# Kernel optimization log

Hardware: AMD Instinct MI355X
Metric: run time of the kernel (lower is better)

The kernel has to match this reference:

```python
import jax, jax.numpy as jnp
from jax import lax
import numpy as np
import math

B = 8
DIFF_LEN, HORIZON, NUM_NODES = 336, 96, 1024
SEG_LEN, D_CONV, D_MODEL = 8, 64, 128
NUM_KERNELS, DEPTH, ALPHA = 6, 2, 0.05
FREQ = math.ceil(DIFF_LEN / SEG_LEN)      # 42
STEP = math.ceil(HORIZON / SEG_LEN)       # 12
PAD = SEG_LEN * FREQ - DIFF_LEN           # 0 here, code stays general
MAXK = 2 * NUM_KERNELS - 1                # 11


def setup_inputs() -> dict:
    key = jax.random.key(0)
    ks = iter(jax.random.split(key, 64))
    p = lambda *s: 0.02 * jax.random.normal(next(ks), s, jnp.float32)
    inp = dict(
        x_diff=jax.random.normal(next(ks), (B, DIFF_LEN, NUM_NODES), jnp.float32),
        adj=jax.random.uniform(next(ks), (NUM_NODES, NUM_NODES), jnp.float32),
        enc_w1=p(SEG_LEN, D_MODEL), enc_b1=p(D_MODEL),
        enc_w2=p(D_MODEL, D_CONV), enc_b2=p(D_CONV),
        dec_w1=p(D_CONV, D_MODEL), dec_b1=p(D_MODEL),
        dec_w2=p(D_MODEL, SEG_LEN), dec_b2=p(SEG_LEN),
        g1_w=p((DEPTH + 1) * D_CONV, D_CONV), g1_b=p(D_CONV),
        g2_w=p((DEPTH + 1) * D_CONV, D_CONV), g2_b=p(D_CONV),
    )
    for i in range(NUM_KERNELS):
        inp[f'conv_w{i}'] = p(D_CONV, D_CONV, 1, 2 * i + 1)
        inp[f'conv_b{i}'] = p(D_CONV)
    return inp


def _mlp(x, w1, b1, w2, b2):
    # 2-hidden-layer MLP with ReLU (dropout = identity at eval)
    return jnp.maximum(x @ w1 + b1, 0.0) @ w2 + b2


def _t_inception(x, conv_ws, conv_bs):
    # x: (B, D, N, T); inception = mean of 'same'-padded (1, 2i+1) convs
    out = jnp.zeros_like(x)
    for i, (w, b) in enumerate(zip(conv_ws, conv_bs)):
        out = out + lax.conv_general_dilated(
            x, w, (1, 1), ((0, 0), (i, i)),
            dimension_numbers=('NCHW', 'OIHW', 'NCHW')) + b[None, :, None, None]
    return out / len(conv_ws)


def _norm_adj(adj):
    a = adj + jnp.eye(adj.shape[0], dtype=adj.dtype)
    return a / a.sum(1, keepdims=True)


def _mixprop(x, a, w, b):
    # x: (B, T, N, D), a: row-normalized (N, N)
    h = x
    outs = [h]
    for _ in range(DEPTH):
        h = ALPHA * x + (1.0 - ALPHA) * jnp.einsum('vn,btnd->btvd', a, h)
        outs.append(h)
    return jnp.concatenate(outs, -1) @ w + b


def _stconv(x, a1, a2, conv_ws, conv_bs, g1_w, g1_b, g2_w, g2_b):
    res = jnp.transpose(x, (0, 3, 2, 1))            # b d n t
    res = _t_inception(res, conv_ws, conv_bs)
    res = jnp.transpose(res, (0, 3, 2, 1))          # b t n d
    res = _mixprop(res, a1, g1_w, g1_b) + _mixprop(res, a2, g2_w, g2_b)
    return res + x                                   # dropout = identity at eval


def reference(x_diff, adj,
              enc_w1, enc_b1, enc_w2, enc_b2,
              dec_w1, dec_b1, dec_w2, dec_b2,
              g1_w, g1_b, g2_w, g2_b,
              conv_w0, conv_b0, conv_w1, conv_b1, conv_w2, conv_b2,
              conv_w3, conv_b3, conv_w4, conv_b4, conv_w5, conv_b5):
    conv_ws = [conv_w0, conv_w1, conv_w2, conv_w3, conv_w4, conv_w5]
    conv_bs = [conv_b0, conv_b1, conv_b2, conv_b3, conv_b4, conv_b5]
    Bb, L, N = x_diff.shape
    a1 = _norm_adj(adj)
    a2 = _norm_adj(adj.T)

    # segment + left-pad with tail so length = FREQ * SEG_LEN
    res = jnp.concatenate((x_diff[:, L - PAD:, :], x_diff), axis=1)
    res = res.reshape(Bb, FREQ, SEG_LEN, N)
    res = jnp.transpose(res, (0, 1, 3, 2))          # (B, F, N, P)
    res = _mlp(res, enc_w1, enc_b1, enc_w2, enc_b2)  # (B, F, N, D)

    # reconstruction branch (teacher-forced one-step shift)
    rec = jnp.concatenate(
        (res[:, :1],
         _stconv(res[:, :-1], a1, a2, conv_ws, conv_bs, g1_w, g1_b, g2_w, g2_b)),
        axis=1)
    rec = _mlp(rec, dec_w1, dec_b1, dec_w2, dec_b2)  # (B, F, N, P)
    rec = jnp.transpose(rec, (0, 1, 3, 2)).reshape(Bb, FREQ * SEG_LEN, N)
    rec = rec[:, -DIFF_LEN:, :]

    cur = res[:, -MAXK:]                             # (B, MAXK, N, D)
    preds = []
    for _ in range(STEP):
        p = _stconv(cur, a1, a2, conv_ws, conv_bs, g1_w, g1_b, g2_w, g2_b)[:, -1:]
        preds.append(p)
        cur = jnp.concatenate((cur[:, 1:], p), axis=1)
    pred = jnp.concatenate(preds, axis=1)            # (B, STEP, N, D)
    pred = _mlp(pred, dec_w1, dec_b1, dec_w2, dec_b2)  # (B, STEP, N, SEG)
    # NOTE: original torch code does a raw .reshape (not transpose); replicate it
    pred = pred.reshape(Bb, STEP * SEG_LEN, N)[:, :HORIZON, :]
    return (rec, pred)
```

## Files before the change

### kernel.cpp

```cpp
#include <hip/hip_runtime.h>

typedef __bf16 bf16;
typedef __bf16 bf16x8 __attribute__((ext_vector_type(8)));
typedef float f32x4 __attribute__((ext_vector_type(4)));

#define N_NODES 1024
#define DC 64
#define FREQ 42
#define TREC 41
#define NB 8
#define MAXK 11
#define NSTEP 12
#define SLICE 65536

__global__ void transpose_k(const float* __restrict__ in, float* __restrict__ out) {
  __shared__ float tile[32][33];
  int bx = blockIdx.x * 32, by = blockIdx.y * 32;
  int x = threadIdx.x, y = threadIdx.y;
#pragma unroll
  for (int j = 0; j < 32; j += 8) tile[y + j][x] = in[(size_t)(by + y + j) * N_NODES + bx + x];
  __syncthreads();
#pragma unroll
  for (int j = 0; j < 32; j += 8) out[(size_t)(bx + y + j) * N_NODES + by + x] = tile[x][y + j];
}

__global__ void rowsum_k(const float* __restrict__ m, float* __restrict__ sums) {
  int v = blockIdx.x;
  float s = 0.f;
  for (int n = threadIdx.x; n < N_NODES; n += 256) s += m[(size_t)v * N_NODES + n];
  __shared__ float red[256];
  red[threadIdx.x] = s;
  __syncthreads();
  for (int w = 128; w > 0; w >>= 1) {
    if (threadIdx.x < w) red[threadIdx.x] += red[threadIdx.x + w];
    __syncthreads();
  }
  if (threadIdx.x == 0) sums[v] = red[0] + 1.0f;
}

__global__ void norm_k(const float* __restrict__ adj, const float* __restrict__ adjT,
                       const float* __restrict__ rs, const float* __restrict__ cs,
                       bf16* __restrict__ a1, bf16* __restrict__ a2) {
  int v = blockIdx.x & (N_NODES - 1);
  bool second = blockIdx.x >= N_NODES;
  const float* src = second ? adjT : adj;
  float inv = 1.0f / (second ? cs[v] : rs[v]);
  bf16* dst = second ? a2 : a1;
  for (int n = threadIdx.x; n < N_NODES; n += 256) {
    float val = src[(size_t)v * N_NODES + n] + (n == v ? 1.0f : 0.0f);
    dst[(size_t)v * N_NODES + n] = (bf16)(val * inv);
  }
}

__global__ __launch_bounds__(256) void btrans_k(const bf16* __restrict__ src,
                                                bf16* __restrict__ dst) {
  __shared__ __align__(16) bf16 t[64][72];
  int bx = blockIdx.x * 64, by = blockIdx.y * 64;
  int tid = threadIdx.x;
#pragma unroll
  for (int i = 0; i < 2; ++i) {
    int q = tid + i * 256;
    int r = q >> 3, c = (q & 7) * 8;
    *(uint4*)&t[r][c] = *(const uint4*)&src[(size_t)(by + r) * N_NODES + bx + c];
  }
  __syncthreads();
#pragma unroll
  for (int i = 0; i < 2; ++i) {
    int q = tid + i * 256;
    int rr = q >> 3, cc = (q & 7) * 8;
    bf16 tmp[8];
#pragma unroll
    for (int e = 0; e < 8; ++e) tmp[e] = t[cc + e][rr];
    *(uint4*)&dst[(size_t)(bx + rr) * N_NODES + by + cc] = *(uint4*)tmp;
  }
}

__global__ void combine_w_k(const float* w0, const float* w1, const float* w2, const float* w3,
                            const float* w4, const float* w5, const float* b0, const float* b1,
                            const float* b2, const float* b3, const float* b4, const float* b5,
                            bf16* __restrict__ Wc, float* __restrict__ bsum) {
  int idx = blockIdx.x * 256 + threadIdx.x;
  if (idx < MAXK * 4096) {
    int dtI = idx >> 12;
    int dout = (idx >> 6) & 63;
    int di = idx & 63;
    int d = dtI - 5;
    int ad = d < 0 ? -d : d;
    const float* ws[6] = {w0, w1, w2, w3, w4, w5};
    float s = 0.f;
    for (int i = 0; i < 6; ++i)
      if (i >= ad) {
        int K = 2 * i + 1;
        s += ws[i][((size_t)dout * 64 + di) * K + (d + i)];
      }
    Wc[idx] = (bf16)s;
  }
  if (idx < 64) bsum[idx] = b0[idx] + b1[idx] + b2[idx] + b3[idx] + b4[idx] + b5[idx];
}

__global__ void vt_k(const float* __restrict__ g1w, const float* __restrict__ g2w,
                     const float* __restrict__ g1b, const float* __restrict__ g2b,
                     bf16* __restrict__ Vt, float* __restrict__ gbsum) {
  int idx = blockIdx.x * 256 + threadIdx.x;
  if (idx < 64) gbsum[idx] = g1b[idx] + g2b[idx];
  if (idx >= 5 * 4096) return;
  int j = idx >> 12;
  int dout = (idx >> 6) & 63;
  int din = idx & 63;
  const float al = 0.05f, bt = 0.95f;
  float v;
  if (j == 0)
    v = g1w[din * 64 + dout] + g2w[din * 64 + dout] +
        al * (g1w[(64 + din) * 64 + dout] + g1w[(128 + din) * 64 + dout] +
              g2w[(64 + din) * 64 + dout] + g2w[(128 + din) * 64 + dout]);
  else if (j == 1)
    v = bt * g1w[(64 + din) * 64 + dout] + al * bt * g1w[(128 + din) * 64 + dout];
  else if (j == 2)
    v = bt * bt * g1w[(128 + din) * 64 + dout];
  else if (j == 3)
    v = bt * g2w[(64 + din) * 64 + dout] + al * bt * g2w[(128 + din) * 64 + dout];
  else
    v = bt * bt * g2w[(128 + din) * 64 + dout];
  Vt[idx] = (bf16)v;
}

__global__ void prep_misc_k(const float* __restrict__ w2, const float* __restrict__ dw1,
                            const float* __restrict__ dw2, bf16* __restrict__ w2T,
                            bf16* __restrict__ dw1b, bf16* __restrict__ dw1T,
                            bf16* __restrict__ dw2T) {
  int i = blockIdx.x * 256 + threadIdx.x;
  if (i < 8192) {
    int dout = i >> 7, j = i & 127;
    w2T[i] = (bf16)w2[(size_t)j * 64 + dout];
    dw1b[i] = (bf16)dw1[i];
    int jj = i >> 6, k = i & 63;
    dw1T[i] = (bf16)dw1[k * 128 + jj];
  }
  if (i < 2048) {
    int s = i >> 7, j = i & 127;
    dw2T[i] = (s < 8) ? (bf16)dw2[j * 8 + s] : (bf16)0.f;
  }
}

__global__ __launch_bounds__(256) void encoder_k(const float* __restrict__ x,
                                                 const float* __restrict__ w1,
                                                 const float* __restrict__ b1,
                                                 const bf16* __restrict__ w2T,
                                                 const float* __restrict__ b2,
                                                 bf16* __restrict__ resb) {
  __shared__ __align__(16) float xs[8 * 64];
  __shared__ __align__(16) float w1s[8 * 128];
  __shared__ float b1s[128];
  __shared__ float b2s[64];
  __shared__ __align__(16) bf16 hA[64 * 136];
  __shared__ __align__(16) bf16 wB[64 * 136];
  int tid = threadIdx.x;
  int v0 = blockIdx.x * 64;
  int bfp = blockIdx.y;
  int b = bfp / FREQ, f = bfp % FREQ;
#pragma unroll
  for (int i = 0; i < 2; ++i) {
    int q = tid + i * 256;
    xs[q] = x[(size_t)(b * 336 + f * 8 + (q >> 6)) * 1024 + v0 + (q & 63)];
  }
#pragma unroll
  for (int i = 0; i < 4; ++i) {
    int q = tid + i * 256;
    w1s[q] = w1[q];
  }
#pragma unroll
  for (int i = 0; i < 4; ++i) {
    int q = tid + i * 256;
    int dout = q >> 4, jc = (q & 15) * 8;
    *(uint4*)&wB[dout * 136 + jc] = *(const uint4*)&w2T[dout * 128 + jc];
  }
  if (tid < 128) b1s[tid] = b1[tid];
  if (tid < 64) b2s[tid] = b2[tid];
  __syncthreads();
  {
    int n = tid & 63, jc = (tid >> 6) * 32;
    for (int jj = 0; jj < 32; ++jj) {
      int j = jc + jj;
      float a = b1s[j];
#pragma unroll
      for (int k = 0; k < 8; ++k) a = fmaf(xs[k * 64 + n], w1s[k * 128 + j], a);
      hA[n * 136 + j] = (bf16)fmaxf(a, 0.f);
    }
  }
  __syncthreads();
  int wid = tid >> 6, lane = tid & 63, lr = lane & 15, lg = lane >> 4;
  f32x4 acc[4] = {};
#pragma unroll
  for (int ks = 0; ks < 4; ++ks) {
    bf16x8 a = *(const bf16x8*)&hA[(wid * 16 + lr) * 136 + ks * 32 + lg * 8];
#pragma unroll
    for (int ni = 0; ni < 4; ++ni) {
      bf16x8 bb = *(const bf16x8*)&wB[(ni * 16 + lr) * 136 + ks * 32 + lg * 8];
      acc[ni] = __builtin_amdgcn_mfma_f32_16x16x32_bf16(a, bb, acc[ni], 0, 0, 0);
    }
  }
  __syncthreads();
#pragma unroll
  for (int ni = 0; ni < 4; ++ni) {
    int n = ni * 16 + lr;
    float bz = b2s[n];
#pragma unroll
    for (int r = 0; r < 4; ++r) wB[(wid * 16 + lg * 4 + r) * 72 + n] = (bf16)(acc[ni][r] + bz);
  }
  __syncthreads();
  size_t so = (size_t)(b * FREQ + f) * SLICE;
#pragma unroll
  for (int i = 0; i < 2; ++i) {
    int q = tid + i * 256;
    int r = q >> 3, c = (q & 7) * 8;
    *(uint4*)&resb[so + (size_t)(v0 + r) * 64 + c] = *(uint4*)&wB[r * 72 + c];
  }
}

__global__ void curinit_k(const bf16* __restrict__ resb, float* __restrict__ cur,
                          bf16* __restrict__ curb) {
  size_t idx = (size_t)blockIdx.x * 256 + threadIdx.x;
  const size_t per_b = (size_t)MAXK * SLICE;
  if (idx < (size_t)NB * per_b) {
    size_t b = idx / per_b, rem = idx % per_b;
    bf16 v = resb[b * ((size_t)FREQ * SLICE) + (size_t)31 * SLICE + rem];
    cur[idx] = (float)v;
    curb[idx] = v;
  }
}

__device__ __forceinline__ void stageA(bf16* lds_a, const bf16* src, int rowStride, int tid) {
#pragma unroll
  for (int i = 0; i < 8; ++i) {
    int q = tid + i * 256;
    int r = q >> 3, c = (q & 7) << 3;
    *(uint4*)&lds_a[r * 72 + c] = *(const uint4*)&src[(size_t)r * rowStride + c];
  }
}
__device__ __forceinline__ void stageB(bf16* lds_b, const bf16* src, int rowStride, int tid) {
#pragma unroll
  for (int i = 0; i < 2; ++i) {
    int q = tid + i * 256;
    int r = q >> 3, c = (q & 7) << 3;
    *(uint4*)&lds_b[r * 72 + c] = *(const uint4*)&src[(size_t)r * rowStride + c];
  }
}
__device__ __forceinline__ void mfma64(const bf16* lds_a, const bf16* lds_b, int wid, int lane,
                                       f32x4 acc[4][4]) {
  int lr = lane & 15, lg = lane >> 4;
#pragma unroll
  for (int h = 0; h < 2; ++h) {
    bf16x8 af[4], bfr[4];
#pragma unroll
    for (int mi = 0; mi < 4; ++mi)
      af[mi] = *(const bf16x8*)&lds_a[(wid * 64 + mi * 16 + lr) * 72 + h * 32 + lg * 8];
#pragma unroll
    for (int ni = 0; ni < 4; ++ni)
      bfr[ni] = *(const bf16x8*)&lds_b[(ni * 16 + lr) * 72 + h * 32 + lg * 8];
#pragma unroll
    for (int mi = 0; mi < 4; ++mi)
#pragma unroll
      for (int ni = 0; ni < 4; ++ni)
        acc[mi][ni] =
            __builtin_amdgcn_mfma_f32_16x16x32_bf16(af[mi], bfr[ni], acc[mi][ni], 0, 0, 0);
  }
}

__global__ __launch_bounds__(256) void asq_k(const bf16* __restrict__ a,
                                             const bf16* __restrict__ aT,
                                             bf16* __restrict__ out) {
  __shared__ __align__(16) bf16 As[64 * 72];
  __shared__ __align__(16) bf16 Bs2[64 * 72];
  int tid = threadIdx.x, w = tid >> 6, lane = tid & 63;
  int lr = lane & 15, lg = lane >> 4;
  int v0 = blockIdx.x * 64, n0 = blockIdx.y * 64;
  f32x4 acc[4] = {};
  for (int k0 = 0; k0 < 1024; k0 += 64) {
    __syncthreads();
    stageB(As, a + (size_t)v0 * 1024 + k0, 1024, tid);
    stageB(Bs2, aT + (size_t)n0 * 1024 + k0, 1024, tid);
    __syncthreads();
#pragma unroll
    for (int h = 0; h < 2; ++h) {
      bf16x8 av = *(const bf16x8*)&As[(w * 16 + lr) * 72 + h * 32 + lg * 8];
#pragma unroll
      for (int ni = 0; ni < 4; ++ni) {
        bf16x8 bv = *(const bf16x8*)&Bs2[(ni * 16 + lr) * 72 + h * 32 + lg * 8];
        acc[ni] = __builtin_amdgcn_mfma_f32_16x16x32_bf16(av, bv, acc[ni], 0, 0, 0);
      }
    }
  }
#pragma unroll
  for (int ni = 0; ni < 4; ++ni)
#pragma unroll
    for (int r = 0; r < 4; ++r) As[(w * 16 + lg * 4 + r) * 72 + ni * 16 + lr] = (bf16)acc[ni][r];
  __syncthreads();
#pragma unroll
  for (int i = 0; i < 2; ++i) {
    int q = tid + i * 256;
    int r = q >> 3, c = (q & 7) * 8;
    *(uint4*)&out[(size_t)(v0 + r) * 1024 + n0 + c] = *(uint4*)&As[r * 72 + c];
  }
}

__global__ __launch_bounds__(256) void incep_k(const bf16* __restrict__ resb, int b0,
                                               const bf16* __restrict__ Wc,
                                               const float* __restrict__ bsum,
                                               bf16* __restrict__ xcN, bf16* __restrict__ xcF) {
  __shared__ __align__(16) bf16 lds_a[256 * 72];
  __shared__ __align__(16) bf16 lds_b[64 * 72];
  int tid = threadIdx.x, wid = tid >> 6, lane = tid & 63;
  int v0 = blockIdx.x * 256;
  int sl = blockIdx.y;
  int b = b0 + sl / TREC, tt = sl % TREC;
  f32x4 acc[4][4] = {};
  for (int dt = 0; dt < MAXK; ++dt) {
    int ts = tt + dt - 5;
    if (ts < 0 || ts >= TREC) continue;
    __syncthreads();
    stageA(lds_a, resb + (size_t)(b * FREQ + ts) * SLICE + (size_t)v0 * 64, 64, tid);
    stageB(lds_b, Wc + dt * 4096, 64, tid);
    __syncthreads();
    mfma64(lds_a, lds_b, wid, lane, acc);
  }
  int lr = lane & 15, lg = lane >> 4;
  size_t so = (size_t)sl * SLICE;
#pragma unroll
  for (int mi = 0; mi < 4; ++mi)
#pragma unroll
    for (int ni = 0; ni < 4; ++ni) {
      int n = ni * 16 + lr;
      float bs = bsum[n];
      union { bf16 h[4]; uint2 u; } pk;
#pragma unroll
      for (int r = 0; r < 4; ++r) {
        int m = wid * 64 + mi * 16 + lg * 4 + r;
        bf16 bv = (bf16)((acc[mi][ni][r] + bs) * (1.f / 6.f));
        lds_a[m * 72 + n] = bv;
        pk.h[r] = bv;
      }
      *(uint2*)&xcF[so + (size_t)n * 1024 + v0 + wid * 64 + mi * 16 + lg * 4] = pk.u;
    }
  __syncthreads();
#pragma unroll
  for (int i = 0; i < 8; ++i) {
    int q = tid + i * 256;
    int r = q >> 3, c = (q & 7) * 8;
    *(uint4*)&xcN[so + (size_t)(v0 + r) * 64 + c] = *(uint4*)&lds_a[r * 72 + c];
  }
}

__global__ __launch_bounds__(256) void fusedrec_k(
    const bf16* __restrict__ xcN, const bf16* __restrict__ xcF, const bf16* __restrict__ a1,
    const bf16* __restrict__ a1q, const bf16* __restrict__ a2, const bf16* __restrict__ a2q,
    const bf16* __restrict__ Vt, const float* __restrict__ gbsum,
    const bf16* __restrict__ resb, int b0, const bf16* __restrict__ dw1T,
    const float* __restrict__ db1, const bf16* __restrict__ dw2T,
    const float* __restrict__ db2, float* __restrict__ outRec) {
  __shared__ __align__(16) bf16 reg1[4][64 * 72];
  __shared__ __align__(16) bf16 reg2[64 * 72];
  __shared__ __align__(16) bf16 valb[64 * 72];
  bf16* hb = &reg1[0][0];
  int tid = threadIdx.x, w = tid >> 6, lane = tid & 63;
  int lr = lane & 15, lg = lane >> 4;
  int v0 = blockIdx.x * 64;
  int sy = blockIdx.y;
  int bl = sy / FREQ, f = sy % FREQ;
  int b = b0 + bl;

  if (f == 0) {
    const bf16* src = resb + (size_t)(b * FREQ) * SLICE + (size_t)v0 * 64;
#pragma unroll
    for (int i = 0; i < 2; ++i) {
      int q = tid + i * 256;
      int r = q >> 3, c = (q & 7) * 8;
      *(uint4*)&valb[r * 72 + c] = *(const uint4*)&src[(size_t)r * 64 + c];
    }
    __syncthreads();
  } else {
    int tt = f - 1;
    size_t so = (size_t)(bl * TREC + tt) * SLICE;
    f32x4 acc[4][4] = {};
    for (int k0 = 0; k0 < 1024; k0 += 64) {
      __syncthreads();
#pragma unroll
      for (int i = 0; i < 8; ++i) {
        int q = tid + i * 256;
        int mm = q >> 9, pos = q & 511;
        int rr = pos >> 3, cc = (pos & 7) * 8;
        const bf16* mp = mm == 0 ? a1 : (mm == 1 ? a1q : (mm == 2 ? a2 : a2q));
        *(uint4*)&reg1[mm][rr * 72 + cc] = *(const uint4*)&mp[(size_t)(v0 + rr) * 1024 + k0 + cc];
      }
#pragma unroll
      for (int i = 0; i < 2; ++i) {
        int q = tid + i * 256;
        int rb = q >> 3, cbb = (q & 7) * 8;
        *(uint4*)&reg2[rb * 72 + cbb] = *(const uint4*)&xcF[so + (size_t)rb * 1024 + k0 + cbb];
      }
      __syncthreads();
#pragma unroll
      for (int h = 0; h < 2; ++h) {
        bf16x8 af[4], bfr[4];
#pragma unroll
        for (int mi = 0; mi < 4; ++mi)
          af[mi] = *(const bf16x8*)&reg1[w][(mi * 16 + lr) * 72 + h * 32 + lg * 8];
#pragma unroll
        for (int ni = 0; ni < 4; ++ni)
          bfr[ni] = *(const bf16x8*)&reg2[(ni * 16 + lr) * 72 + h * 32 + lg * 8];
#pragma unroll
        for (int mi = 0; mi < 4; ++mi)
#pragma unroll
          for (int ni = 0; ni < 4; ++ni)
            acc[mi][ni] =
                __builtin_amdgcn_mfma_f32_16x16x32_bf16(af[mi], bfr[ni], acc[mi][ni], 0, 0, 0);
      }
    }
    __syncthreads();
#pragma unroll
    for (int mi = 0; mi < 4; ++mi)
#pragma unroll
      for (int ni = 0; ni < 4; ++ni)
#pragma unroll
        for (int r = 0; r < 4; ++r)
          reg1[w][(mi * 16 + lg * 4 + r) * 72 + ni * 16 + lr] = (bf16)acc[mi][ni][r];
#pragma unroll
    for (int i = 0; i < 2; ++i) {
      int q = tid + i * 256;
      int r = q >> 3, c = (q & 7) * 8;
      *(uint4*)&reg2[r * 72 + c] = *(const uint4*)&xcN[so + (size_t)(v0 + r) * 64 + c];
    }
    __syncthreads();
    f32x4 z[4] = {};
#pragma unroll
    for (int j = 0; j < 5; ++j) {
      const bf16* Asrc = (j == 0) ? reg2 : &reg1[j - 1][0];
#pragma unroll
      for (int h = 0; h < 2; ++h) {
        bf16x8 a = *(const bf16x8*)&Asrc[(w * 16 + lr) * 72 + h * 32 + lg * 8];
#pragma unroll
        for (int ni = 0; ni < 4; ++ni) {
          bf16x8 bb =
              *(const bf16x8*)&Vt[(size_t)j * 4096 + (ni * 16 + lr) * 64 + h * 32 + lg * 8];
          z[ni] = __builtin_amdgcn_mfma_f32_16x16x32_bf16(a, bb, z[ni], 0, 0, 0);
        }
      }
    }
    const bf16* xb = resb + (size_t)(b * FREQ + tt) * SLICE + (size_t)v0 * 64;
#pragma unroll
    for (int ni = 0; ni < 4; ++ni) {
      int n = ni * 16 + lr;
      float gb = gbsum[n];
#pragma unroll
      for (int r = 0; r < 4; ++r) {
        int m = w * 16 + lg * 4 + r;
        valb[m * 72 + n] = (bf16)((float)xb[(size_t)m * 64 + n] + z[ni][r] + gb);
      }
    }
    __syncthreads();
  }
  f32x4 hacc[4][2] = {};
#pragma unroll
  for (int h = 0; h < 2; ++h) {
    bf16x8 a[4];
#pragma unroll
    for (int mi = 0; mi < 4; ++mi)
      a[mi] = *(const bf16x8*)&valb[(mi * 16 + lr) * 72 + h * 32 + lg * 8];
#pragma unroll
    for (int ni2 = 0; ni2 < 2; ++ni2) {
      bf16x8 bb = *(const bf16x8*)&dw1T[(w * 32 + ni2 * 16 + lr) * 64 + h * 32 + lg * 8];
#pragma unroll
      for (int mi = 0; mi < 4; ++mi)
        hacc[mi][ni2] = __builtin_amdgcn_mfma_f32_16x16x32_bf16(a[mi], bb, hacc[mi][ni2], 0, 0, 0);
    }
  }
  __syncthreads();
#pragma unroll
  for (int ni2 = 0; ni2 < 2; ++ni2) {
    int j = w * 32 + ni2 * 16 + lr;
    float bz = db1[j];
#pragma unroll
    for (int mi = 0; mi < 4; ++mi)
#pragma unroll
      for (int r = 0; r < 4; ++r)
        hb[(mi * 16 + lg * 4 + r) * 136 + j] = (bf16)fmaxf(hacc[mi][ni2][r] + bz, 0.f);
  }
  __syncthreads();
  f32x4 oacc = {};
#pragma unroll
  for (int kc = 0; kc < 4; ++kc) {
    bf16x8 a = *(const bf16x8*)&hb[(w * 16 + lr) * 136 + kc * 32 + lg * 8];
    bf16x8 bb = *(const bf16x8*)&dw2T[lr * 128 + kc * 32 + lg * 8];
    oacc = __builtin_amdgcn_mfma_f32_16x16x32_bf16(a, bb, oacc, 0, 0, 0);
  }
  if (lr < 8) {
    float bz = db2[lr];
    float4 o;
    o.x = oacc[0] + bz;
    o.y = oacc[1] + bz;
    o.z = oacc[2] + bz;
    o.w = oacc[3] + bz;
    *(float4*)&outRec[(size_t)b * 344064 + (size_t)(f * 8 + lr) * 1024 + v0 + w * 16 + lg * 4] =
        o;
  }
}

__device__ __forceinline__ void arrive_wait(unsigned* c, int tid) {
  __syncthreads();
  if (tid == 0) {
    __hip_atomic_fetch_add(c, 1u, __ATOMIC_RELAXED, __HIP_MEMORY_SCOPE_AGENT);
    while (__hip_atomic_load(c, __ATOMIC_RELAXED, __HIP_MEMORY_SCOPE_AGENT) < 64u)
      __builtin_amdgcn_s_sleep(2);
  }
  __syncthreads();
}

__device__ __forceinline__ void incep16(const bf16* __restrict__ curb,
                                        const bf16* __restrict__ Wc, const float* bsums_,
                                        int base, int b, int r0, int w, int lr, int lg,
                                        bf16* yL, bf16* yFdst) {
  f32x4 ya = {};
  for (int j = 0; j < 6; ++j) {
    int slot = (base + 5 + j) % MAXK;
    const bf16* cb = curb + ((size_t)b * MAXK + slot) * SLICE + (size_t)r0 * 64;
#pragma unroll
    for (int h = 0; h < 2; ++h) {
      bf16x8 a = *(const bf16x8*)&cb[lr * 64 + h * 32 + lg * 8];
      bf16x8 bb = *(const bf16x8*)&Wc[(size_t)j * 4096 + (w * 16 + lr) * 64 + h * 32 + lg * 8];
      ya = __builtin_amdgcn_mfma_f32_16x16x32_bf16(a, bb, ya, 0, 0, 0);
    }
  }
  int n = w * 16 + lr;
  float bs = bsums_[n];
  union { bf16 h[4]; unsigned long long u; } pk;
#pragma unroll
  for (int r = 0; r < 4; ++r) {
    int m = lg * 4 + r;
    bf16 bv = (bf16)((ya[r] + bs) * (1.f / 6.f));
    yL[m * 72 + n] = bv;
    pk.h[r] = bv;
  }
  __hip_atomic_store((unsigned long long*)(yFdst + (size_t)n * 1024 + r0 + lg * 4), pk.u,
                     __ATOMIC_RELAXED, __HIP_MEMORY_SCOPE_AGENT);
}

struct AR4 {
  const bf16 *Wc;
  const float *bsum;
  const bf16 *a1, *a1q, *a2, *a2q;
  const bf16 *Vt;
  const float *gbsum;
  float *cur;
  bf16 *curb;
  bf16 *yF;
  const bf16 *dw1b;
  const float *db1, *dw2, *db2;
  float *outPred;
  unsigned *bar;
};

__global__ void __launch_bounds__(256) ar4_k(AR4 p) {
  __shared__ __align__(16) bf16 As4[4][16 * 72];
  __shared__ __align__(16) bf16 Bs[64 * 72];
  __shared__ __align__(16) bf16 yL[16 * 72];
  __shared__ __align__(16) bf16 PL[4][16 * 72];
  __shared__ __align__(16) bf16 dw1s[8192];
  __shared__ float dw2s[1024];
  __shared__ float db1s[128], db2s[8], bsums[64], gbsums[64];
  __shared__ __align__(16) float val[16 * 68];
  __shared__ __align__(16) bf16 hs[16 * 136];
  int tid = threadIdx.x, w = tid >> 6, lane = tid & 63;
  int lr = lane & 15, lg = lane >> 4;
  int bid = blockIdx.x, b = bid >> 6, l = bid & 63;
  unsigned* cnt = p.bar + b * 32;
  int r0 = l * 16;

#pragma unroll
  for (int i = 0; i < 4; ++i) {
    int q = tid + i * 256;
    *(uint4*)&dw1s[q * 8] = *(const uint4*)&p.dw1b[q * 8];
    dw2s[q] = p.dw2[q];
  }
  if (tid < 128) db1s[tid] = p.db1[tid];
  if (tid < 8) db2s[tid] = p.db2[tid];
  if (tid < 64) {
    bsums[tid] = p.bsum[tid];
    gbsums[tid] = p.gbsum[tid];
  }
  __syncthreads();

  incep16(p.curb, p.Wc, bsums, 0, b, r0, w, lr, lg, yL, p.yF + (size_t)b * SLICE);
  arrive_wait(cnt + 0, tid);

  const bf16* mats[4] = {p.a1, p.a1q, p.a2, p.a2q};
  for (int s = 0; s < NSTEP; ++s) {
    {
      const bf16* yFs = p.yF + ((size_t)s * NB + b) * SLICE;
      f32x4 acc[4] = {};
      for (int k0 = 0; k0 < 1024; k0 += 64) {
        __syncthreads();
#pragma unroll
        for (int i = 0; i < 2; ++i) {
          int q = tid + i * 256;
          int mm = q >> 7, rr = (q >> 3) & 15, cc = (q & 7) * 8;
          *(uint4*)&As4[mm][rr * 72 + cc] =
              *(const uint4*)&mats[mm][(size_t)(r0 + rr) * 1024 + k0 + cc];
          int rb = q >> 3, cb2 = (q & 7) * 8;
          *(uint4*)&Bs[rb * 72 + cb2] = *(const uint4*)&yFs[(size_t)rb * 1024 + k0 + cb2];
        }
        __syncthreads();
#pragma unroll
        for (int h = 0; h < 2; ++h) {
          bf16x8 a = *(const bf16x8*)&As4[w][lr * 72 + h * 32 + lg * 8];
#pragma unroll
          for (int ni = 0; ni < 4; ++ni) {
            bf16x8 bb = *(const bf16x8*)&Bs[(ni * 16 + lr) * 72 + h * 32 + lg * 8];
            acc[ni] = __builtin_amdgcn_mfma_f32_16x16x32_bf16(a, bb, acc[ni], 0, 0, 0);
          }
        }
      }
#pragma unroll
      for (int ni = 0; ni < 4; ++ni) {
        int nn = ni * 16 + lr;
#pragma unroll
        for (int r = 0; r < 4; ++r) PL[w][(lg * 4 + r) * 72 + nn] = (bf16)acc[ni][r];
      }
    }
    __syncthreads();
    {
      f32x4 z = {};
#pragma unroll
      for (int j = 0; j < 5; ++j) {
        const bf16* Aj = (j == 0) ? yL : PL[j - 1];
#pragma unroll
        for (int h = 0; h < 2; ++h) {
          bf16x8 a = *(const bf16x8*)&Aj[lr * 72 + h * 32 + lg * 8];
          bf16x8 bb =
              *(const bf16x8*)&p.Vt[(size_t)j * 4096 + (w * 16 + lr) * 64 + h * 32 + lg * 8];
          z = __builtin_amdgcn_mfma_f32_16x16x32_bf16(a, bb, z, 0, 0, 0);
        }
      }
      int slotR = (s + 10) % MAXK, slotW = s % MAXK;
      size_t xo = ((size_t)b * MAXK + slotR) * SLICE + (size_t)r0 * 64;
      size_t wo = ((size_t)b * MAXK + slotW) * SLICE + (size_t)r0 * 64;
      int n = w * 16 + lr;
      float gb = gbsums[n];
#pragma unroll
      for (int r = 0; r < 4; ++r) {
        int m = lg * 4 + r;
        size_t o = (size_t)m * 64 + n;
        float v = p.cur[xo + o] + z[r] + gb;
        p.cur[wo + o] = v;
        p.curb[wo + o] = (bf16)v;
        val[m * 68 + n] = v;
      }
      __syncthreads();
      if (s < NSTEP - 1)
        incep16(p.curb, p.Wc, bsums, s + 1, b, r0, w, lr, lg, yL,
                p.yF + ((size_t)(s + 1) * NB + b) * SLICE);
      {
        int j = tid & 127, rblk = tid >> 7;
        for (int rr2 = 0; rr2 < 8; ++rr2) {
          int m = rblk * 8 + rr2;
          float a = db1s[j];
#pragma unroll 16
          for (int k = 0; k < 64; ++k) a = fmaf(val[m * 68 + k], (float)dw1s[k * 128 + j], a);
          hs[m * 136 + j] = (bf16)fmaxf(a, 0.f);
        }
      }
      __syncthreads();
      if (tid < 128) {
        int m = tid >> 3, sg = tid & 7;
        float a = db2s[sg];
#pragma unroll 16
        for (int j2 = 0; j2 < 128; ++j2)
          a = fmaf((float)hs[m * 136 + j2], dw2s[j2 * 8 + sg], a);
        p.outPred[(size_t)b * 98304 + (size_t)s * 8192 + (size_t)(r0 + m) * 8 + sg] = a;
      }
    }
    if (s < NSTEP - 1) arrive_wait(cnt + 1 + s, tid);
  }
}

extern "C" void kernel_launch(void* const* d_in, const int* in_sizes, int n_in, void* d_out,
                              int out_size, void* d_ws, size_t ws_size, hipStream_t stream) {
  const float* x_diff = (const float*)d_in[0];
  const float* adj = (const float*)d_in[1];
  const float* enc_w1 = (const float*)d_in[2];
  const float* enc_b1 = (const float*)d_in[3];
  const float* enc_w2 = (const float*)d_in[4];
  const float* enc_b2 = (const float*)d_in[5];
  const float* dec_w1 = (const float*)d_in[6];
  const float* dec_b1 = (const float*)d_in[7];
  const float* dec_w2 = (const float*)d_in[8];
  const float* dec_b2 = (const float*)d_in[9];
  const float* g1_w = (const float*)d_in[10];
  const float* g1_b = (const float*)d_in[11];
  const float* g2_w = (const float*)d_in[12];
  const float* g2_b = (const float*)d_in[13];
  const float* cw[6];
  const float* cb_[6];
  for (int i = 0; i < 6; ++i) {
    cw[i] = (const float*)d_in[14 + 2 * i];
    cb_[i] = (const float*)d_in[15 + 2 * i];
  }

  char* base = (char*)d_ws;
  size_t off = 0;
  auto alloc = [&](size_t bytes) -> void* {
    void* p = base + off;
    off = (off + bytes + 255) & ~(size_t)255;
    return p;
  };
  float* adjT = (float*)alloc(1048576ULL * 4);
  float* rowsum = (float*)alloc(4096);
  float* colsum = (float*)alloc(4096);
  bf16* a1b = (bf16*)alloc(1048576ULL * 2);
  bf16* a2b = (bf16*)alloc(1048576ULL * 2);
  bf16* a1T = (bf16*)alloc(1048576ULL * 2);
  bf16* a2T = (bf16*)alloc(1048576ULL * 2);
  bf16* a1q = (bf16*)alloc(1048576ULL * 2);
  bf16* a2q = (bf16*)alloc(1048576ULL * 2);
  bf16* Wc = (bf16*)alloc(45056ULL * 2);
  float* bsum = (float*)alloc(256);
  float* gbsum = (float*)alloc(256);
  bf16* Vt = (bf16*)alloc(20480ULL * 2);
  bf16* w2T = (bf16*)alloc(8192ULL * 2);
  bf16* dw1b = (bf16*)alloc(8192ULL * 2);
  bf16* dw1T = (bf16*)alloc(8192ULL * 2);
  bf16* dw2T = (bf16*)alloc(2048ULL * 2);
  bf16* resb = (bf16*)alloc((size_t)NB * FREQ * SLICE * 2);
  float* cur = (float*)alloc((size_t)NB * MAXK * SLICE * 4);
  bf16* curb = (bf16*)alloc((size_t)NB * MAXK * SLICE * 2);
  bf16* yF = (bf16*)alloc((size_t)NSTEP * NB * SLICE * 2);
  unsigned* gbar = (unsigned*)alloc(4096);
  size_t fixedEnd = off;
  int cb = NB;
  while (cb > 1) {
    size_t S = (size_t)TREC * cb;
    if (fixedEnd + S * SLICE * 4 + 65536 <= ws_size) break;
    cb >>= 1;
  }
  size_t S = (size_t)TREC * cb;
  bf16* xcN = (bf16*)alloc(S * SLICE * 2);
  bf16* xcF = (bf16*)alloc(S * SLICE * 2);

  float* outF = (float*)d_out;
  float* outRec = outF;
  float* outPred = outF + (size_t)2752512;

  transpose_k<<<dim3(32, 32), dim3(32, 8), 0, stream>>>(adj, adjT);
  rowsum_k<<<1024, 256, 0, stream>>>(adj, rowsum);
  rowsum_k<<<1024, 256, 0, stream>>>(adjT, colsum);
  norm_k<<<2048, 256, 0, stream>>>(adj, adjT, rowsum, colsum, a1b, a2b);
  btrans_k<<<dim3(16, 16), 256, 0, stream>>>(a1b, a1T);
  btrans_k<<<dim3(16, 16), 256, 0, stream>>>(a2b, a2T);
  asq_k<<<dim3(16, 16), 256, 0, stream>>>(a1b, a1T, a1q);
  asq_k<<<dim3(16, 16), 256, 0, stream>>>(a2b, a2T, a2q);
  combine_w_k<<<(MAXK * 4096 + 255) / 256, 256, 0, stream>>>(cw[0], cw[1], cw[2], cw[3], cw[4],
                                                             cw[5], cb_[0], cb_[1], cb_[2],
                                                             cb_[3], cb_[4], cb_[5], Wc, bsum);
  vt_k<<<80, 256, 0, stream>>>(g1_w, g2_w, g1_b, g2_b, Vt, gbsum);
  prep_misc_k<<<32, 256, 0, stream>>>(enc_w2, dec_w1, dec_w2, w2T, dw1b, dw1T, dw2T);
  encoder_k<<<dim3(16, NB * FREQ), 256, 0, stream>>>(x_diff, enc_w1, enc_b1, w2T, enc_b2,
                                                     resb);
  curinit_k<<<(int)(((size_t)NB * MAXK * SLICE + 255) / 256), 256, 0, stream>>>(resb, cur,
                                                                                curb);

  for (int c0 = 0; c0 < NB; c0 += cb) {
    int Sg = TREC * cb;
    incep_k<<<dim3(4, Sg), 256, 0, stream>>>(resb, c0, Wc, bsum, xcN, xcF);
    fusedrec_k<<<dim3(16, cb * FREQ), 256, 0, stream>>>(xcN, xcF, a1b, a1q, a2b, a2q, Vt,
                                                        gbsum, resb, c0, dw1T, dec_b1, dw2T,
                                                        dec_b2, outRec);
  }

  hipMemsetAsync(gbar, 0, 4096, stream);
  AR4 arp;
  arp.Wc = Wc; arp.bsum = bsum;
  arp.a1 = a1b; arp.a1q = a1q; arp.a2 = a2b; arp.a2q = a2q;
  arp.Vt = Vt; arp.gbsum = gbsum;
  arp.cur = cur; arp.curb = curb;
  arp.yF = yF;
  arp.dw1b = dw1b; arp.db1 = dec_b1; arp.dw2 = dec_w2; arp.db2 = dec_b2;
  arp.outPred = outPred;
  arp.bar = gbar;
  ar4_k<<<dim3(512), dim3(256), 0, stream>>>(arp);
}
```

Baseline: 889.5 us.

## Load MFMA operands directly from global memory and use MFMA for decoder MLP

The inception, fused reconstruction and autoregressive kernels now feed MFMA fragments straight from global memory instead of staging tiles through LDS with barriers. This removes the per-k-step __syncthreads and LDS traffic, and shrinks shared memory. The autoregressive kernel's per-step decoder MLP moves from scalar FMA loops over fp32 values to bf16 MFMA using the pre-transposed weights, and the barrier spin sleep is lengthened. Direct global loads may be poorly coalesced and rely on cache hits, and the decoder input is now rounded to bf16, which changes precision.

After: 1.567 ms. 76.2% more time.

```diff
diff --git a/kernel.cpp b/kernel.cpp
--- a/kernel.cpp
+++ b/kernel.cpp
@@ -126,13 +126,11 @@
 
 __global__ void prep_misc_k(const float* __restrict__ w2, const float* __restrict__ dw1,
                             const float* __restrict__ dw2, bf16* __restrict__ w2T,
-                            bf16* __restrict__ dw1b, bf16* __restrict__ dw1T,
-                            bf16* __restrict__ dw2T) {
+                            bf16* __restrict__ dw1T, bf16* __restrict__ dw2T) {
   int i = blockIdx.x * 256 + threadIdx.x;
   if (i < 8192) {
     int dout = i >> 7, j = i & 127;
     w2T[i] = (bf16)w2[(size_t)j * 64 + dout];
-    dw1b[i] = (bf16)dw1[i];
     int jj = i >> 6, k = i & 63;
     dw1T[i] = (bf16)dw1[k * 128 + jj];
   }
@@ -229,40 +227,12 @@
   }
 }
 
-__device__ __forceinline__ void stageA(bf16* lds_a, const bf16* src, int rowStride, int tid) {
-#pragma unroll
-  for (int i = 0; i < 8; ++i) {
-    int q = tid + i * 256;
-    int r = q >> 3, c = (q & 7) << 3;
-    *(uint4*)&lds_a[r * 72 + c] = *(const uint4*)&src[(size_t)r * rowStride + c];
-  }
-}
 __device__ __forceinline__ void stageB(bf16* lds_b, const bf16* src, int rowStride, int tid) {
 #pragma unroll
   for (int i = 0; i < 2; ++i) {
     int q = tid + i * 256;
     int r = q >> 3, c = (q & 7) << 3;
     *(uint4*)&lds_b[r * 72 + c] = *(const uint4*)&src[(size_t)r * rowStride + c];
-  }
-}
-__device__ __forceinline__ void mfma64(const bf16* lds_a, const bf16* lds_b, int wid, int lane,
-                                       f32x4 acc[4][4]) {
-  int lr = lane & 15, lg = lane >> 4;
-#pragma unroll
-  for (int h = 0; h < 2; ++h) {
-    bf16x8 af[4], bfr[4];
-#pragma unroll
-    for (int mi = 0; mi < 4; ++mi)
-      af[mi] = *(const bf16x8*)&lds_a[(wid * 64 + mi * 16 + lr) * 72 + h * 32 + lg * 8];
-#pragma unroll
-    for (int ni = 0; ni < 4; ++ni)
-      bfr[ni] = *(const bf16x8*)&lds_b[(ni * 16 + lr) * 72 + h * 32 + lg * 8];
-#pragma unroll
-    for (int mi = 0; mi < 4; ++mi)
-#pragma unroll
-      for (int ni = 0; ni < 4; ++ni)
-        acc[mi][ni] =
-            __builtin_amdgcn_mfma_f32_16x16x32_bf16(af[mi], bfr[ni], acc[mi][ni], 0, 0, 0);
   }
 }
 
@@ -307,9 +277,9 @@
                                                const bf16* __restrict__ Wc,
                                                const float* __restrict__ bsum,
                                                bf16* __restrict__ xcN, bf16* __restrict__ xcF) {
-  __shared__ __align__(16) bf16 lds_a[256 * 72];
-  __shared__ __align__(16) bf16 lds_b[64 * 72];
+  __shared__ __align__(16) bf16 lds_t[256 * 72];
   int tid = threadIdx.x, wid = tid >> 6, lane = tid & 63;
+  int lr = lane & 15, lg = lane >> 4;
   int v0 = blockIdx.x * 256;
   int sl = blockIdx.y;
   int b = b0 + sl / TREC, tt = sl % TREC;
@@ -317,13 +287,26 @@
   for (int dt = 0; dt < MAXK; ++dt) {
     int ts = tt + dt - 5;
     if (ts < 0 || ts >= TREC) continue;
-    __syncthreads();
-    stageA(lds_a, resb + (size_t)(b * FREQ + ts) * SLICE + (size_t)v0 * 64, 64, tid);
-    stageB(lds_b, Wc + dt * 4096, 64, tid);
-    __syncthreads();
-    mfma64(lds_a, lds_b, wid, lane, acc);
-  }
-  int lr = lane & 15, lg = lane >> 4;
+    const bf16* src = resb + (size_t)(b * FREQ + ts) * SLICE;
+    const bf16* wc = Wc + dt * 4096;
+#pragma unroll
+    for (int h = 0; h < 2; ++h) {
+      bf16x8 af[4], bfr[4];
+#pragma unroll
+      for (int mi = 0; mi < 4; ++mi)
+        af[mi] = *(const bf16x8*)&src[(size_t)(v0 + wid * 64 + mi * 16 + lr) * 64 + h * 32 +
+                                      lg * 8];
+#pragma unroll
+      for (int ni = 0; ni < 4; ++ni)
+        bfr[ni] = *(const bf16x8*)&wc[(ni * 16 + lr) * 64 + h * 32 + lg * 8];
+#pragma unroll
+      for (int mi = 0; mi < 4; ++mi)
+#pragma unroll
+        for (int ni = 0; ni < 4; ++ni)
+          acc[mi][ni] =
+              __builtin_amdgcn_mfma_f32_16x16x32_bf16(af[mi], bfr[ni], acc[mi][ni], 0, 0, 0);
+    }
+  }
   size_t so = (size_t)sl * SLICE;
 #pragma unroll
   for (int mi = 0; mi < 4; ++mi)
@@ -336,7 +319,7 @@
       for (int r = 0; r < 4; ++r) {
         int m = wid * 64 + mi * 16 + lg * 4 + r;
         bf16 bv = (bf16)((acc[mi][ni][r] + bs) * (1.f / 6.f));
-        lds_a[m * 72 + n] = bv;
+        lds_t[m * 72 + n] = bv;
         pk.h[r] = bv;
       }
       *(uint2*)&xcF[so + (size_t)n * 1024 + v0 + wid * 64 + mi * 16 + lg * 4] = pk.u;
@@ -346,7 +329,7 @@
   for (int i = 0; i < 8; ++i) {
     int q = tid + i * 256;
     int r = q >> 3, c = (q & 7) * 8;
-    *(uint4*)&xcN[so + (size_t)(v0 + r) * 64 + c] = *(uint4*)&lds_a[r * 72 + c];
+    *(uint4*)&xcN[so + (size_t)(v0 + r) * 64 + c] = *(uint4*)&lds_t[r * 72 + c];
   }
 }
 
@@ -380,33 +363,20 @@
   } else {
     int tt = f - 1;
     size_t so = (size_t)(bl * TREC + tt) * SLICE;
+    const bf16* mp = w == 0 ? a1 : (w == 1 ? a1q : (w == 2 ? a2 : a2q));
     f32x4 acc[4][4] = {};
     for (int k0 = 0; k0 < 1024; k0 += 64) {
-      __syncthreads();
-#pragma unroll
-      for (int i = 0; i < 8; ++i) {
-        int q = tid + i * 256;
-        int mm = q >> 9, pos = q & 511;
-        int rr = pos >> 3, cc = (pos & 7) * 8;
-        const bf16* mp = mm == 0 ? a1 : (mm == 1 ? a1q : (mm == 2 ? a2 : a2q));
-        *(uint4*)&reg1[mm][rr * 72 + cc] = *(const uint4*)&mp[(size_t)(v0 + rr) * 1024 + k0 + cc];
-      }
-#pragma unroll
-      for (int i = 0; i < 2; ++i) {
-        int q = tid + i * 256;
-        int rb = q >> 3, cbb = (q & 7) * 8;
-        *(uint4*)&reg2[rb * 72 + cbb] = *(const uint4*)&xcF[so + (size_t)rb * 1024 + k0 + cbb];
-      }
-      __syncthreads();
 #pragma unroll
       for (int h = 0; h < 2; ++h) {
         bf16x8 af[4], bfr[4];
 #pragma unroll
         for (int mi = 0; mi < 4; ++mi)
-          af[mi] = *(const bf16x8*)&reg1[w][(mi * 16 + lr) * 72 + h * 32 + lg * 8];
+          af[mi] =
+              *(const bf16x8*)&mp[(size_t)(v0 + mi * 16 + lr) * 1024 + k0 + h * 32 + lg * 8];
 #pragma unroll
         for (int ni = 0; ni < 4; ++ni)
-          bfr[ni] = *(const bf16x8*)&reg2[(ni * 16 + lr) * 72 + h * 32 + lg * 8];
+          bfr[ni] =
+              *(const bf16x8*)&xcF[so + (size_t)(ni * 16 + lr) * 1024 + k0 + h * 32 + lg * 8];
 #pragma unroll
         for (int mi = 0; mi < 4; ++mi)
 #pragma unroll
@@ -415,7 +385,6 @@
                 __builtin_amdgcn_mfma_f32_16x16x32_bf16(af[mi], bfr[ni], acc[mi][ni], 0, 0, 0);
       }
     }
-    __syncthreads();
 #pragma unroll
     for (int mi = 0; mi < 4; ++mi)
 #pragma unroll
@@ -509,7 +478,7 @@
   if (tid == 0) {
     __hip_atomic_fetch_add(c, 1u, __ATOMIC_RELAXED, __HIP_MEMORY_SCOPE_AGENT);
     while (__hip_atomic_load(c, __ATOMIC_RELAXED, __HIP_MEMORY_SCOPE_AGENT) < 64u)
-      __builtin_amdgcn_s_sleep(2);
+      __builtin_amdgcn_s_sleep(8);
   }
   __syncthreads();
 }
@@ -543,7 +512,7 @@
                      __ATOMIC_RELAXED, __HIP_MEMORY_SCOPE_AGENT);
 }
 
-struct AR4 {
+struct AR5 {
   const bf16 *Wc;
   const float *bsum;
   const bf16 *a1, *a1q, *a2, *a2q;
@@ -552,34 +521,26 @@
   float *cur;
   bf16 *curb;
   bf16 *yF;
-  const bf16 *dw1b;
-  const float *db1, *dw2, *db2;
+  const bf16 *dw1T;
+  const float *db1;
+  const bf16 *dw2T;
+  const float *db2;
   float *outPred;
   unsigned *bar;
 };
 
-__global__ void __launch_bounds__(256) ar4_k(AR4 p) {
-  __shared__ __align__(16) bf16 As4[4][16 * 72];
-  __shared__ __align__(16) bf16 Bs[64 * 72];
+__global__ void __launch_bounds__(256) ar5_k(AR5 p) {
   __shared__ __align__(16) bf16 yL[16 * 72];
   __shared__ __align__(16) bf16 PL[4][16 * 72];
-  __shared__ __align__(16) bf16 dw1s[8192];
-  __shared__ float dw2s[1024];
+  __shared__ __align__(16) bf16 valb[16 * 72];
+  __shared__ __align__(16) bf16 hb[16 * 136];
   __shared__ float db1s[128], db2s[8], bsums[64], gbsums[64];
-  __shared__ __align__(16) float val[16 * 68];
-  __shared__ __align__(16) bf16 hs[16 * 136];
   int tid = threadIdx.x, w = tid >> 6, lane = tid & 63;
   int lr = lane & 15, lg = lane >> 4;
   int bid = blockIdx.x, b = bid >> 6, l = bid & 63;
   unsigned* cnt = p.bar + b * 32;
   int r0 = l * 16;
 
-#pragma unroll
-  for (int i = 0; i < 4; ++i) {
-    int q = tid + i * 256;
-    *(uint4*)&dw1s[q * 8] = *(const uint4*)&p.dw1b[q * 8];
-    dw2s[q] = p.dw2[q];
-  }
   if (tid < 128) db1s[tid] = p.db1[tid];
   if (tid < 8) db2s[tid] = p.db2[tid];
   if (tid < 64) {
@@ -591,29 +552,21 @@
   incep16(p.curb, p.Wc, bsums, 0, b, r0, w, lr, lg, yL, p.yF + (size_t)b * SLICE);
   arrive_wait(cnt + 0, tid);
 
-  const bf16* mats[4] = {p.a1, p.a1q, p.a2, p.a2q};
+  const bf16* mats_w = w == 0 ? p.a1 : (w == 1 ? p.a1q : (w == 2 ? p.a2 : p.a2q));
+  const bf16* Arow = mats_w + (size_t)r0 * 1024;
   for (int s = 0; s < NSTEP; ++s) {
     {
       const bf16* yFs = p.yF + ((size_t)s * NB + b) * SLICE;
       f32x4 acc[4] = {};
+#pragma unroll 2
       for (int k0 = 0; k0 < 1024; k0 += 64) {
-        __syncthreads();
-#pragma unroll
-        for (int i = 0; i < 2; ++i) {
-          int q = tid + i * 256;
-          int mm = q >> 7, rr = (q >> 3) & 15, cc = (q & 7) * 8;
-          *(uint4*)&As4[mm][rr * 72 + cc] =
-              *(const uint4*)&mats[mm][(size_t)(r0 + rr) * 1024 + k0 + cc];
-          int rb = q >> 3, cb2 = (q & 7) * 8;
-          *(uint4*)&Bs[rb * 72 + cb2] = *(const uint4*)&yFs[(size_t)rb * 1024 + k0 + cb2];
-        }
-        __syncthreads();
 #pragma unroll
         for (int h = 0; h < 2; ++h) {
-          bf16x8 a = *(const bf16x8*)&As4[w][lr * 72 + h * 32 + lg * 8];
+          bf16x8 a = *(const bf16x8*)&Arow[(size_t)lr * 1024 + k0 + h * 32 + lg * 8];
 #pragma unroll
           for (int ni = 0; ni < 4; ++ni) {
-            bf16x8 bb = *(const bf16x8*)&Bs[(ni * 16 + lr) * 72 + h * 32 + lg * 8];
+            bf16x8 bb =
+                *(const bf16x8*)&yFs[(size_t)(ni * 16 + lr) * 1024 + k0 + h * 32 + lg * 8];
             acc[ni] = __builtin_amdgcn_mfma_f32_16x16x32_bf16(a, bb, acc[ni], 0, 0, 0);
           }
         }
@@ -651,30 +604,44 @@
         float v = p.cur[xo + o] + z[r] + gb;
         p.cur[wo + o] = v;
         p.curb[wo + o] = (bf16)v;
-        val[m * 68 + n] = v;
+        valb[m * 72 + n] = (bf16)v;
       }
       __syncthreads();
       if (s < NSTEP - 1)
         incep16(p.curb, p.Wc, bsums, s + 1, b, r0, w, lr, lg, yL,
                 p.yF + ((size_t)(s + 1) * NB + b) * SLICE);
-      {
-        int j = tid & 127, rblk = tid >> 7;
-        for (int rr2 = 0; rr2 < 8; ++rr2) {
-          int m = rblk * 8 + rr2;
-          float a = db1s[j];
-#pragma unroll 16
-          for (int k = 0; k < 64; ++k) a = fmaf(val[m * 68 + k], (float)dw1s[k * 128 + j], a);
-          hs[m * 136 + j] = (bf16)fmaxf(a, 0.f);
+      f32x4 hacc[2] = {};
+#pragma unroll
+      for (int h = 0; h < 2; ++h) {
+        bf16x8 a = *(const bf16x8*)&valb[lr * 72 + h * 32 + lg * 8];
+#pragma unroll
+        for (int ni2 = 0; ni2 < 2; ++ni2) {
+          bf16x8 bb = *(const bf16x8*)&p.dw1T[(w * 32 + ni2 * 16 + lr) * 64 + h * 32 + lg * 8];
+          hacc[ni2] = __builtin_amdgcn_mfma_f32_16x16x32_bf16(a, bb, hacc[ni2], 0, 0, 0);
         }
       }
+#pragma unroll
+      for (int ni2 = 0; ni2 < 2; ++ni2) {
+        int j = w * 32 + ni2 * 16 + lr;
+        float bz = db1s[j];
+#pragma unroll
+        for (int r = 0; r < 4; ++r)
+          hb[(lg * 4 + r) * 136 + j] = (bf16)fmaxf(hacc[ni2][r] + bz, 0.f);
+      }
       __syncthreads();
-      if (tid < 128) {
-        int m = tid >> 3, sg = tid & 7;
-        float a = db2s[sg];
-#pragma unroll 16
-        for (int j2 = 0; j2 < 128; ++j2)
-          a = fmaf((float)hs[m * 136 + j2], dw2s[j2 * 8 + sg], a);
-        p.outPred[(size_t)b * 98304 + (size_t)s * 8192 + (size_t)(r0 + m) * 8 + sg] = a;
+      f32x4 oacc = {};
+#pragma unroll
+      for (int kc = 0; kc < 4; ++kc) {
+        bf16x8 a = *(const bf16x8*)&hb[lr * 136 + kc * 32 + lg * 8];
+        bf16x8 bb = *(const bf16x8*)&p.dw2T[lr * 128 + kc * 32 + lg * 8];
+        oacc = __builtin_amdgcn_mfma_f32_16x16x32_bf16(a, bb, oacc, 0, 0, 0);
+      }
+      if (w == 0 && lr < 8) {
+        float bz = db2s[lr];
+#pragma unroll
+        for (int r = 0; r < 4; ++r)
+          p.outPred[(size_t)b * 98304 + (size_t)s * 8192 + (size_t)(r0 + lg * 4 + r) * 8 + lr] =
+              oacc[r] + bz;
       }
     }
     if (s < NSTEP - 1) arrive_wait(cnt + 1 + s, tid);
@@ -725,7 +692,6 @@
   float* gbsum = (float*)alloc(256);
   bf16* Vt = (bf16*)alloc(20480ULL * 2);
   bf16* w2T = (bf16*)alloc(8192ULL * 2);
-  bf16* dw1b = (bf16*)alloc(8192ULL * 2);
   bf16* dw1T = (bf16*)alloc(8192ULL * 2);
   bf16* dw2T = (bf16*)alloc(2048ULL * 2);
   bf16* resb = (bf16*)alloc((size_t)NB * FREQ * SLICE * 2);
@@ -760,7 +726,7 @@
                                                              cw[5], cb_[0], cb_[1], cb_[2],
                                                              cb_[3], cb_[4], cb_[5], Wc, bsum);
   vt_k<<<80, 256, 0, stream>>>(g1_w, g2_w, g1_b, g2_b, Vt, gbsum);
-  prep_misc_k<<<32, 256, 0, stream>>>(enc_w2, dec_w1, dec_w2, w2T, dw1b, dw1T, dw2T);
+  prep_misc_k<<<32, 256, 0, stream>>>(enc_w2, dec_w1, dec_w2, w2T, dw1T, dw2T);
   encoder_k<<<dim3(16, NB * FREQ), 256, 0, stream>>>(x_diff, enc_w1, enc_b1, w2T, enc_b2,
                                                      resb);
   curinit_k<<<(int)(((size_t)NB * MAXK * SLICE + 255) / 256), 256, 0, stream>>>(resb, cur,
@@ -775,14 +741,14 @@
   }
 
   hipMemsetAsync(gbar, 0, 4096, stream);
-  AR4 arp;
+  AR5 arp;
   arp.Wc = Wc; arp.bsum = bsum;
   arp.a1 = a1b; arp.a1q = a1q; arp.a2 = a2b; arp.a2q = a2q;
   arp.Vt = Vt; arp.gbsum = gbsum;
   arp.cur = cur; arp.curb = curb;
   arp.yF = yF;
-  arp.dw1b = dw1b; arp.db1 = dec_b1; arp.dw2 = dec_w2; arp.db2 = dec_b2;
+  arp.dw1T = dw1T; arp.db1 = dec_b1; arp.dw2T = dw2T; arp.db2 = dec_b2;
   arp.outPred = outPred;
   arp.bar = gbar;
-  ar4_k<<<dim3(512), dim3(256), 0, stream>>>(arp);
-}
+  ar5_k<<<dim3(512), dim3(256), 0, stream>>>(arp);
+}
```
